# Kernel tuning notes

Hardware: AMD Instinct MI355X
Metric: run time of the kernel (lower is better)

The kernel has to match this reference:

```python
import jax, jax.numpy as jnp
import numpy as np

EMBED_DIM = 768
NUM_HEADS = 12
NUM_BOND_TYPES = 4
NEG_INF = -1e9


def setup_inputs() -> dict:
    key = jax.random.key(0)
    ks = jax.random.split(key, 8)
    B, N, E = 32, 512, EMBED_DIM
    x = jax.random.normal(ks[0], (B, N, E), dtype=jnp.float32)
    adj = jax.random.randint(ks[1], (B, N, N), 0, 2, dtype=jnp.int32)
    bond = jax.random.randint(ks[2], (B, N, N), 0, NUM_BOND_TYPES + 1, dtype=jnp.int32)
    # nn.Linear(E, 3E): weight (3E, E), bias (3E)
    lim_qkv = 1.0 / np.sqrt(E)
    qkv_w = jax.random.uniform(ks[3], (3 * E, E), minval=-lim_qkv, maxval=lim_qkv, dtype=jnp.float32)
    qkv_b = jax.random.uniform(ks[4], (3 * E,), minval=-lim_qkv, maxval=lim_qkv, dtype=jnp.float32)
    out_w = jax.random.uniform(ks[5], (E, E), minval=-lim_qkv, maxval=lim_qkv, dtype=jnp.float32)
    out_b = jax.random.uniform(ks[6], (E,), minval=-lim_qkv, maxval=lim_qkv, dtype=jnp.float32)
    # nn.Embedding(num_bond_types+1, 1), padding_idx=0 -> row 0 is zero
    bond_table = jax.random.normal(ks[7], (NUM_BOND_TYPES + 1, 1), dtype=jnp.float32)
    bond_table = bond_table.at[0].set(0.0)
    return {"x": x, "adj": adj, "bond": bond, "num_heads": NUM_HEADS,
            "qkv_w": qkv_w, "qkv_b": qkv_b, "out_w": out_w, "out_b": out_b,
            "bond_table": bond_table}


def reference(x, adj, bond, num_heads, qkv_w, qkv_b, out_w, out_b, bond_table):
    B, N, E = x.shape
    hd = E // num_heads
    scale = hd ** -0.5
    # enforce padding_idx=0 semantics
    bond_table = bond_table.at[0].set(0.0)
    qkv = x @ qkv_w.T + qkv_b                      # (B, N, 3E)
    qkv = qkv.reshape(B, N, 3, num_heads, hd).transpose(2, 0, 3, 1, 4)
    q, k, v = qkv[0], qkv[1], qkv[2]               # (B, h, N, hd)
    attn = jnp.einsum('bhnd,bhmd->bhnm', q, k) * scale
    attn = attn + adj.astype(x.dtype)[:, None, :, :]
    bond_bias = bond_table[bond, 0]                # (B, N, N) embedding gather
    attn = attn + bond_bias[:, None, :, :]
    attn = jnp.where(attn == 0, NEG_INF, attn)     # masked_fill(attn == 0)
    attn = jax.nn.softmax(attn, axis=-1)
    out = jnp.einsum('bhnm,bhmd->bhnd', attn, v)   # (B, h, N, hd)
    out = out.transpose(0, 2, 1, 3).reshape(B, N, E)
    return out @ out_w.T + out_b
```

## Files before the change

kernel.cpp:

```cpp
#include <hip/hip_runtime.h>
#include <hip/hip_bf16.h>

typedef __attribute__((ext_vector_type(8))) short short8;
typedef __attribute__((ext_vector_type(4))) float f32x4;
typedef __attribute__((ext_vector_type(4))) unsigned int uint4v;
typedef __attribute__((ext_vector_type(4))) int int4v;

#define MFMA16(a,b,c) __builtin_amdgcn_mfma_f32_16x16x32_bf16((a),(b),(c),0,0,0)

#define GLOAD_LDS16(g, l) \
    __builtin_amdgcn_global_load_lds((const __attribute__((address_space(1))) void*)(g), \
                                     (__attribute__((address_space(3))) void*)(l), 16, 0, 0)

__device__ __forceinline__ unsigned short f2bf(float f){
    union { float f; unsigned int u; } c; c.f = f;
    unsigned int u = c.u;
    u = (u + 0x7fffu + ((u >> 16) & 1u)) >> 16;
    return (unsigned short)u;
}
__device__ __forceinline__ float bf2f(unsigned short s){
    union { unsigned int u; float f; } c; c.u = ((unsigned int)s) << 16;
    return c.f;
}

__device__ __forceinline__ unsigned int pack_split(float f){
    unsigned int u = __builtin_bit_cast(unsigned int, f);
    float hi = __builtin_bit_cast(float, u & 0xffff0000u);
    unsigned int rem = __builtin_bit_cast(unsigned int, f - hi);
    return __builtin_amdgcn_perm(rem, u, 0x07060302u);
}

__device__ __forceinline__ void unpack8(uint4v u0, uint4v u1, short8& hi, short8& lo){
    uint4v h, l;
    h[0] = __builtin_amdgcn_perm(u0[1], u0[0], 0x05040100u);
    h[1] = __builtin_amdgcn_perm(u0[3], u0[2], 0x05040100u);
    h[2] = __builtin_amdgcn_perm(u1[1], u1[0], 0x05040100u);
    h[3] = __builtin_amdgcn_perm(u1[3], u1[2], 0x05040100u);
    l[0] = __builtin_amdgcn_perm(u0[1], u0[0], 0x07060302u);
    l[1] = __builtin_amdgcn_perm(u0[3], u0[2], 0x07060302u);
    l[2] = __builtin_amdgcn_perm(u1[1], u1[0], 0x07060302u);
    l[3] = __builtin_amdgcn_perm(u1[3], u1[2], 0x07060302u);
    hi = __builtin_bit_cast(short8, h);
    lo = __builtin_bit_cast(short8, l);
}

__global__ void pack_x_kernel(const float* __restrict__ x, unsigned int* __restrict__ img){
    int tid = blockIdx.x * 256 + threadIdx.x;
    int m = tid / 192, k4 = (tid - m*192) * 4;
    f32x4 v = *(const f32x4*)(x + (size_t)m*768 + k4);
    uint4v p;
    #pragma unroll
    for (int j = 0; j < 4; ++j) p[j] = pack_split(v[j]);
    int mt = m >> 7, row = m & 127, kt = k4 >> 5, u = k4 & 31;
    size_t off = ((size_t)(mt*24 + kt))*16384 + row*128 + (size_t)((u*4) ^ ((row&7)<<4));
    *(uint4v*)((char*)img + off) = p;
}

__global__ void pack_w_kernel(const float* __restrict__ wsrc, unsigned int* __restrict__ img, int total){
    int tid = blockIdx.x * 256 + threadIdx.x;
    if (tid >= total) return;
    int n = tid / 192, k4 = (tid - n*192) * 4;
    f32x4 v = *(const f32x4*)(wsrc + (size_t)n*768 + k4);
    uint4v p;
    #pragma unroll
    for (int j = 0; j < 4; ++j){
        unsigned short hh = f2bf(v[j]);
        unsigned short ll = f2bf(v[j] - bf2f(hh));
        p[j] = (unsigned int)hh | ((unsigned int)ll << 16);
    }
    int jt = n >> 7, row = n & 127, kt = k4 >> 5, u = k4 & 31;
    size_t off = ((size_t)(jt*24 + kt))*16384 + row*128 + (size_t)((u*4) ^ ((row&7)<<4));
    *(uint4v*)((char*)img + off) = p;
}

__global__ void bias_kernel(const int* __restrict__ adj, const int* __restrict__ bond,
                            const float* __restrict__ table, float* __restrict__ biasC, int n4){
    int i = blockIdx.x * 256 + threadIdx.x;
    if (i >= n4) return;
    int4v a  = ((const int4v*)adj)[i];
    int4v bd = ((const int4v*)bond)[i];
    const float t1 = table[1], t2 = table[2], t3 = table[3], t4 = table[4];
    f32x4 o;
    #pragma unroll
    for (int j = 0; j < 4; ++j){
        int bv = bd[j];
        float tb = (bv == 1) ? t1 : (bv == 2) ? t2 : (bv == 3) ? t3 : (bv == 4) ? t4 : 0.0f;
        o[j] = (float)a[j] + tb;
    }
    ((f32x4*)biasC)[i] = o;
}

template<int EMODE>
__global__ __launch_bounds__(256, 3)
void gemm_img(const unsigned int* __restrict__ Aimg, const unsigned int* __restrict__ Bimg,
              const float* __restrict__ bias, int NT, int RPX,
              float* __restrict__ C, int N,
              unsigned int* __restrict__ qo, unsigned int* __restrict__ ko,
              unsigned int* __restrict__ vo)
{
    __shared__ unsigned int lds[8192];

    const int lin = blockIdx.x;
    const int xcd = lin & 7, idx = lin >> 3;
    const int grp  = idx / (RPX * 6);
    const int rem  = idx - grp * (RPX * 6);
    const int rowL = rem / 6, c6 = rem - rowL * 6;
    const int colT = grp * 6 + c6;
    const int mt = xcd * RPX + rowL;
    const int m0 = mt << 7, j0 = colT << 7;

    const int t = threadIdx.x, l = t & 63, w = t >> 6;
    const int c = l & 15, g = l >> 4;
    const int wr = (w >> 1) * 64, wc2 = (w & 1) * 64;

    const unsigned int* Ablk = Aimg + (size_t)mt   * NT * 4096;
    const unsigned int* Bblk = Bimg + (size_t)colT * NT * 4096;

    f32x4 acc[4][4] = {};

    for (int kt = 0; kt < NT; ++kt){
        const unsigned int* As = Ablk + kt*4096 + t*4;
        const unsigned int* Bs = Bblk + kt*4096 + t*4;
        unsigned int* Ad = lds + t*4;
        unsigned int* Bd = lds + 4096 + t*4;
        #pragma unroll
        for (int i = 0; i < 4; ++i){
            GLOAD_LDS16(As + i*1024, Ad + i*1024);
            GLOAD_LDS16(Bs + i*1024, Bd + i*1024);
        }
        __syncthreads();

        short8 bh[4], bl[4];
        #pragma unroll
        for (int fc = 0; fc < 4; ++fc){
            int row = wc2 + fc*16 + c;
            int sw = (row & 7) << 4;
            const char* p = (const char*)(lds + 4096) + row*128;
            uint4v u0 = *(const uint4v*)(p + ((g*32     ) ^ sw));
            uint4v u1 = *(const uint4v*)(p + ((g*32 + 16) ^ sw));
            unpack8(u0, u1, bh[fc], bl[fc]);
        }
        #pragma unroll
        for (int fr = 0; fr < 4; ++fr){
            int row = wr + fr*16 + c;
            int sw = (row & 7) << 4;
            const char* p = (const char*)lds + row*128;
            uint4v u0 = *(const uint4v*)(p + ((g*32     ) ^ sw));
            uint4v u1 = *(const uint4v*)(p + ((g*32 + 16) ^ sw));
            short8 ah, al;
            unpack8(u0, u1, ah, al);
            #pragma unroll
            for (int fc = 0; fc < 4; ++fc){
                acc[fr][fc] = MFMA16(ah, bh[fc], acc[fr][fc]);
                acc[fr][fc] = MFMA16(ah, bl[fc], acc[fr][fc]);
                acc[fr][fc] = MFMA16(al, bh[fc], acc[fr][fc]);
            }
        }
        __syncthreads();
    }

    #pragma unroll
    for (int fr = 0; fr < 4; ++fr){
        #pragma unroll
        for (int fc = 0; fc < 4; ++fc){
            #pragma unroll
            for (int r = 0; r < 4; ++r){
                int m = m0 + wr + fr*16 + g*4 + r;
                int j = j0 + wc2 + fc*16 + c;
                float val = acc[fr][fc][r] + bias[j];
                if constexpr (EMODE == 0){
                    C[(size_t)m * N + j] = val;
                } else {
                    int sec = j / 768;
                    int off = j - sec * 768;
                    int head = off >> 6, d = off & 63;
                    int bb = m >> 9, n = m & 511;
                    unsigned int packed = pack_split(val);
                    if (sec == 2) {
                        vo[(((size_t)bb * 12 + head) * 64 + d) * 512 + n] = packed;
                    } else {
                        unsigned int* dst = (sec == 0) ? qo : ko;
                        dst[(((size_t)bb * 12 + head) * 512 + n) * 64 + d] = packed;
                    }
                }
            }
        }
    }
}

__global__ __launch_bounds__(256, 3)
void attn_kernel(const unsigned int* __restrict__ qb,
                 const unsigned int* __restrict__ kb,
                 const unsigned int* __restrict__ vtb,
                 const float* __restrict__ biasC,
                 unsigned int* __restrict__ oimg)
{
    __shared__ unsigned int Kt[64 * 64];
    __shared__ unsigned int Vt[64 * 64];
    __shared__ unsigned int Pt[4][16 * 68];

    const int lin = blockIdx.x;
    const int xcd = lin & 7, m_ = lin >> 3;
    const int bgrp = m_ / 96, r_ = m_ - bgrp * 96;
    const int b = (bgrp << 3) | xcd;
    const int h = r_ >> 3, qt = r_ & 7;
    const int bh = b * 12 + h, q0 = qt * 64;

    const int t = threadIdx.x, l = t & 63, w = t >> 6;
    const int c = l & 15, g = l >> 4;

    const unsigned int* qp  = qb  + (size_t)bh * 512 * 64;
    const unsigned int* kp  = kb  + (size_t)bh * 512 * 64;
    const unsigned int* vtp = vtb + (size_t)bh * 64 * 512;

    short8 qh[2], ql[2];
    {
        int qrow = q0 + w*16 + c;
        #pragma unroll
        for (int ks = 0; ks < 2; ++ks){
            const unsigned int* p = qp + (size_t)qrow * 64 + ks*32 + g*8;
            uint4v u0 = *(const uint4v*)p;
            uint4v u1 = *(const uint4v*)(p + 4);
            unpack8(u0, u1, qh[ks], ql[ks]);
        }
    }

    f32x4 O[4] = {};
    float mrow[4] = {-3e38f, -3e38f, -3e38f, -3e38f};
    float lrow[4] = {0.f, 0.f, 0.f, 0.f};

    const int srow = t >> 2;
    const int scol = (t & 3) * 16;
    const int ssw  = (srow & 7) << 4;

    auto rdfrag = [&](const unsigned int* base, int row, int colb, short8& hi, short8& lo){
        int sw = (row & 7) << 4;
        const char* p = (const char*)base + row*256;
        uint4v u0 = *(const uint4v*)(p + ((colb     ) ^ sw));
        uint4v u1 = *(const uint4v*)(p + ((colb + 16) ^ sw));
        unpack8(u0, u1, hi, lo);
    };

    for (int kt = 0; kt < 8; ++kt){
        {
            const unsigned int* kg = kp  + (size_t)(kt*64 + srow) * 64 + scol;
            const unsigned int* vg = vtp + (size_t)srow * 512 + kt*64 + scol;
            #pragma unroll
            for (int i = 0; i < 4; ++i){
                uint4v a  = *(const uint4v*)(kg + 4*i);
                uint4v bx = *(const uint4v*)(vg + 4*i);
                int cb = (scol + 4*i) * 4;
                *(uint4v*)((char*)Kt + srow*256 + (cb ^ ssw)) = a;
                *(uint4v*)((char*)Vt + srow*256 + (cb ^ ssw)) = bx;
            }
        }
        __syncthreads();

        float bia[4][4];
        #pragma unroll
        for (int fc = 0; fc < 4; ++fc){
            #pragma unroll
            for (int r = 0; r < 4; ++r){
                int rr = q0 + w*16 + g*4 + r;
                int cc = kt*64 + fc*16 + c;
                bia[fc][r] = biasC[((size_t)b * 512 + rr) * 512 + cc];
            }
        }

        f32x4 S[4] = {};
        #pragma unroll
        for (int fc = 0; fc < 4; ++fc){
            short8 kbh0, kbl0, kbh1, kbl1;
            rdfrag(Kt, fc*16 + c,       g*32, kbh0, kbl0);
            rdfrag(Kt, fc*16 + c, 128 + g*32, kbh1, kbl1);
            __builtin_amdgcn_s_setprio(1);
            S[fc] = MFMA16(qh[0], kbh0, S[fc]);
            S[fc] = MFMA16(qh[0], kbl0, S[fc]);
            S[fc] = MFMA16(ql[0], kbh0, S[fc]);
            S[fc] = MFMA16(qh[1], kbh1, S[fc]);
            S[fc] = MFMA16(qh[1], kbl1, S[fc]);
            S[fc] = MFMA16(ql[1], kbh1, S[fc]);
            __builtin_amdgcn_s_setprio(0);
        }

        float sv[4][4];
        #pragma unroll
        for (int fc = 0; fc < 4; ++fc){
            #pragma unroll
            for (int r = 0; r < 4; ++r){
                float val = fmaf(S[fc][r], 0.125f, bia[fc][r]);
                if (val == 0.0f) val = -1e9f;
                sv[fc][r] = val;
            }
        }

        float pvreg[4][4];
        #pragma unroll
        for (int r = 0; r < 4; ++r){
            float mt = fmaxf(fmaxf(sv[0][r], sv[1][r]), fmaxf(sv[2][r], sv[3][r]));
            #pragma unroll
            for (int off = 1; off < 16; off <<= 1)
                mt = fmaxf(mt, __shfl_xor(mt, off, 16));
            float mn = fmaxf(mrow[r], mt);
            float corr = __expf(mrow[r] - mn);
            float rs = 0.0f;
            #pragma unroll
            for (int fc = 0; fc < 4; ++fc){
                float p = __expf(sv[fc][r] - mn);
                pvreg[fc][r] = p;
                rs += p;
            }
            #pragma unroll
            for (int off = 1; off < 16; off <<= 1)
                rs += __shfl_xor(rs, off, 16);
            lrow[r] = lrow[r] * corr + rs;
            mrow[r] = mn;
            #pragma unroll
            for (int hf = 0; hf < 4; ++hf)
                O[hf][r] *= corr;
        }

        #pragma unroll
        for (int fc = 0; fc < 4; ++fc){
            #pragma unroll
            for (int r = 0; r < 4; ++r){
                Pt[w][(g*4 + r)*68 + fc*16 + c] = pack_split(pvreg[fc][r]);
            }
        }

        #pragma unroll
        for (int ks = 0; ks < 2; ++ks){
            const unsigned int* pp = &Pt[w][c*68 + ks*32 + g*8];
            uint4v pu0 = *(const uint4v*)pp;
            uint4v pu1 = *(const uint4v*)(pp + 4);
            short8 pah, pal;
            unpack8(pu0, pu1, pah, pal);
            #pragma unroll
            for (int hf = 0; hf < 4; ++hf){
                short8 vbh, vbl;
                rdfrag(Vt, hf*16 + c, ks*128 + g*32, vbh, vbl);
                __builtin_amdgcn_s_setprio(1);
                O[hf] = MFMA16(pah, vbh, O[hf]);
                O[hf] = MFMA16(pah, vbl, O[hf]);
                O[hf] = MFMA16(pal, vbh, O[hf]);
                __builtin_amdgcn_s_setprio(0);
            }
        }
        __syncthreads();
    }

    #pragma unroll
    for (int r = 0; r < 4; ++r){
        float inv = 1.0f / lrow[r];
        int m = b*512 + q0 + w*16 + g*4 + r;
        int mt = m >> 7, mrow2 = m & 127;
        int swz = (mrow2 & 7) << 4;
        size_t rowbase = ((size_t)mt*24)*16384 + (size_t)mrow2*128;
        #pragma unroll
        for (int hf = 0; hf < 4; ++hf){
            int e = h*64 + hf*16 + c;
            int kt2 = e >> 5, u = e & 31;
            size_t off = rowbase + (size_t)kt2*16384 + (size_t)((u*4) ^ swz);
            *(unsigned int*)((char*)oimg + off) = pack_split(O[hf][r] * inv);
        }
    }
}

extern "C" void kernel_launch(void* const* d_in, const int* in_sizes, int n_in,
                              void* d_out, int out_size, void* d_ws, size_t ws_size,
                              hipStream_t stream)
{
    const float* x     = (const float*)d_in[0];
    const int*   adj   = (const int*)d_in[1];
    const int*   bond  = (const int*)d_in[2];
    const float* qkv_w = (const float*)d_in[4];
    const float* qkv_b = (const float*)d_in[5];
    const float* out_w = (const float*)d_in[6];
    const float* out_b = (const float*)d_in[7];
    const float* btab  = (const float*)d_in[8];
    float* out = (float*)d_out;

    const size_t QKV = 12582912;
    unsigned int* q   = (unsigned int*)d_ws;
    unsigned int* k   = q  + QKV;
    unsigned int* vt  = k  + QKV;
    unsigned int* r1  = vt + QKV;
    unsigned int* w2i = r1 + QKV;
    unsigned int* r2  = w2i + 589824;
    unsigned int* w1i = r2;
    float* biasC      = (float*)r2;

    dim3 blk(256);
    pack_w_kernel<<<dim3(1728), blk, 0, stream>>>(qkv_w, w1i, 2304*192);
    pack_w_kernel<<<dim3(576),  blk, 0, stream>>>(out_w, w2i, 768*192);
    pack_x_kernel<<<dim3(12288), blk, 0, stream>>>(x, r1);

    gemm_img<1><<<dim3(2304), blk, 0, stream>>>(r1, w1i, qkv_b, 24, 16,
                                                nullptr, 2304, q, k, vt);

    bias_kernel<<<dim3(8192), blk, 0, stream>>>(adj, bond, btab, biasC, (32*512*512)/4);

    attn_kernel<<<dim3(3072), blk, 0, stream>>>(q, k, vt, biasC, r1);

    gemm_img<0><<<dim3(768), blk, 0, stream>>>(r1, w2i, out_b, 24, 16,
                                               out, 768, nullptr, nullptr, nullptr);
}
```

Baseline: 437.1 us.

## Fuse adjacency/bond bias into attention and pre-swizzle K/V tiles for direct LDS loads

Removes the separate bias kernel and its fp32 bias buffer. The attention kernel now reads the adj and bond int arrays directly and does the table lookup inline. The QKV GEMM epilogue writes K and V in a per-64-row tile layout that is already swizzled, so attention can copy them with global_load_lds straight into shared memory instead of going through registers. Each attention block (12 heads × 8 query tiles per batch) re-reads the adj/bond ints, where before it read a precomputed float bias. The total is two int reads per element instead of one float read, plus extra select arithmetic.

```diff
diff --git a/kernel.cpp b/kernel.cpp
--- a/kernel.cpp
+++ b/kernel.cpp
@@ -73,23 +73,6 @@
     *(uint4v*)((char*)img + off) = p;
 }
 
-__global__ void bias_kernel(const int* __restrict__ adj, const int* __restrict__ bond,
-                            const float* __restrict__ table, float* __restrict__ biasC, int n4){
-    int i = blockIdx.x * 256 + threadIdx.x;
-    if (i >= n4) return;
-    int4v a  = ((const int4v*)adj)[i];
-    int4v bd = ((const int4v*)bond)[i];
-    const float t1 = table[1], t2 = table[2], t3 = table[3], t4 = table[4];
-    f32x4 o;
-    #pragma unroll
-    for (int j = 0; j < 4; ++j){
-        int bv = bd[j];
-        float tb = (bv == 1) ? t1 : (bv == 2) ? t2 : (bv == 3) ? t3 : (bv == 4) ? t4 : 0.0f;
-        o[j] = (float)a[j] + tb;
-    }
-    ((f32x4*)biasC)[i] = o;
-}
-
 template<int EMODE>
 __global__ __launch_bounds__(256, 3)
 void gemm_img(const unsigned int* __restrict__ Aimg, const unsigned int* __restrict__ Bimg,
@@ -175,12 +158,18 @@
                     int off = j - sec * 768;
                     int head = off >> 6, d = off & 63;
                     int bb = m >> 9, n = m & 511;
+                    int bh2 = bb * 12 + head;
                     unsigned int packed = pack_split(val);
-                    if (sec == 2) {
-                        vo[(((size_t)bb * 12 + head) * 64 + d) * 512 + n] = packed;
+                    if (sec == 0) {
+                        qo[((size_t)bh2 * 512 + n) * 64 + d] = packed;
+                    } else if (sec == 1) {
+                        int row = n & 63;
+                        ko[(size_t)(bh2*8 + (n>>6))*4096 + row*64
+                           + (((d<<2) ^ ((row&7)<<4)) >> 2)] = packed;
                     } else {
-                        unsigned int* dst = (sec == 0) ? qo : ko;
-                        dst[(((size_t)bb * 12 + head) * 512 + n) * 64 + d] = packed;
+                        int col = n & 63;
+                        vo[(size_t)(bh2*8 + (n>>6))*4096 + d*64
+                           + (((col<<2) ^ ((d&7)<<4)) >> 2)] = packed;
                     }
                 }
             }
@@ -190,13 +179,15 @@
 
 __global__ __launch_bounds__(256, 3)
 void attn_kernel(const unsigned int* __restrict__ qb,
-                 const unsigned int* __restrict__ kb,
-                 const unsigned int* __restrict__ vtb,
-                 const float* __restrict__ biasC,
+                 const unsigned int* __restrict__ kimg,
+                 const unsigned int* __restrict__ vimg,
+                 const int* __restrict__ adj,
+                 const int* __restrict__ bond,
+                 const float* __restrict__ table,
                  unsigned int* __restrict__ oimg)
 {
-    __shared__ unsigned int Kt[64 * 64];
-    __shared__ unsigned int Vt[64 * 64];
+    __shared__ unsigned int Kt[4096];
+    __shared__ unsigned int Vt[4096];
     __shared__ unsigned int Pt[4][16 * 68];
 
     const int lin = blockIdx.x;
@@ -209,9 +200,8 @@
     const int t = threadIdx.x, l = t & 63, w = t >> 6;
     const int c = l & 15, g = l >> 4;
 
-    const unsigned int* qp  = qb  + (size_t)bh * 512 * 64;
-    const unsigned int* kp  = kb  + (size_t)bh * 512 * 64;
-    const unsigned int* vtp = vtb + (size_t)bh * 64 * 512;
+    const unsigned int* qp = qb + (size_t)bh * 512 * 64;
+    const float t1 = table[1], t2 = table[2], t3 = table[3], t4 = table[4];
 
     short8 qh[2], ql[2];
     {
@@ -228,10 +218,6 @@
     f32x4 O[4] = {};
     float mrow[4] = {-3e38f, -3e38f, -3e38f, -3e38f};
     float lrow[4] = {0.f, 0.f, 0.f, 0.f};
-
-    const int srow = t >> 2;
-    const int scol = (t & 3) * 16;
-    const int ssw  = (srow & 7) << 4;
 
     auto rdfrag = [&](const unsigned int* base, int row, int colb, short8& hi, short8& lo){
         int sw = (row & 7) << 4;
@@ -243,29 +229,28 @@
 
     for (int kt = 0; kt < 8; ++kt){
         {
-            const unsigned int* kg = kp  + (size_t)(kt*64 + srow) * 64 + scol;
-            const unsigned int* vg = vtp + (size_t)srow * 512 + kt*64 + scol;
+            const unsigned int* kg = kimg + (size_t)(bh*8 + kt)*4096 + t*4;
+            const unsigned int* vg = vimg + (size_t)(bh*8 + kt)*4096 + t*4;
             #pragma unroll
             for (int i = 0; i < 4; ++i){
-                uint4v a  = *(const uint4v*)(kg + 4*i);
-                uint4v bx = *(const uint4v*)(vg + 4*i);
-                int cb = (scol + 4*i) * 4;
-                *(uint4v*)((char*)Kt + srow*256 + (cb ^ ssw)) = a;
-                *(uint4v*)((char*)Vt + srow*256 + (cb ^ ssw)) = bx;
-            }
-        }
-        __syncthreads();
-
-        float bia[4][4];
+                GLOAD_LDS16(kg + i*1024, &Kt[t*4 + i*1024]);
+                GLOAD_LDS16(vg + i*1024, &Vt[t*4 + i*1024]);
+            }
+        }
+
+        int av[4][4], bv[4][4];
         #pragma unroll
         for (int fc = 0; fc < 4; ++fc){
             #pragma unroll
             for (int r = 0; r < 4; ++r){
                 int rr = q0 + w*16 + g*4 + r;
                 int cc = kt*64 + fc*16 + c;
-                bia[fc][r] = biasC[((size_t)b * 512 + rr) * 512 + cc];
-            }
-        }
+                size_t idx = ((size_t)b * 512 + rr) * 512 + cc;
+                av[fc][r] = adj[idx];
+                bv[fc][r] = bond[idx];
+            }
+        }
+        __syncthreads();
 
         f32x4 S[4] = {};
         #pragma unroll
@@ -288,7 +273,9 @@
         for (int fc = 0; fc < 4; ++fc){
             #pragma unroll
             for (int r = 0; r < 4; ++r){
-                float val = fmaf(S[fc][r], 0.125f, bia[fc][r]);
+                int bb2 = bv[fc][r];
+                float tb = (bb2 == 1) ? t1 : (bb2 == 2) ? t2 : (bb2 == 3) ? t3 : (bb2 == 4) ? t4 : 0.0f;
+                float val = fmaf(S[fc][r], 0.125f, (float)av[fc][r] + tb);
                 if (val == 0.0f) val = -1e9f;
                 sv[fc][r] = val;
             }
@@ -386,9 +373,7 @@
     unsigned int* vt  = k  + QKV;
     unsigned int* r1  = vt + QKV;
     unsigned int* w2i = r1 + QKV;
-    unsigned int* r2  = w2i + 589824;
-    unsigned int* w1i = r2;
-    float* biasC      = (float*)r2;
+    unsigned int* w1i = w2i + 589824;
 
     dim3 blk(256);
     pack_w_kernel<<<dim3(1728), blk, 0, stream>>>(qkv_w, w1i, 2304*192);
@@ -398,9 +383,7 @@
     gemm_img<1><<<dim3(2304), blk, 0, stream>>>(r1, w1i, qkv_b, 24, 16,
                                                 nullptr, 2304, q, k, vt);
 
-    bias_kernel<<<dim3(8192), blk, 0, stream>>>(adj, bond, btab, biasC, (32*512*512)/4);
-
-    attn_kernel<<<dim3(3072), blk, 0, stream>>>(q, k, vt, biasC, r1);
+    attn_kernel<<<dim3(3072), blk, 0, stream>>>(q, k, vt, adj, bond, btab, r1);
 
     gemm_img<0><<<dim3(768), blk, 0, stream>>>(r1, w2i, out_b, 24, 16,
                                                out, 768, nullptr, nullptr, nullptr);
```

Measured after the change: 451.6 us. +3.3%, slower.

## Store bf16 hi/lo planes pre-split in tiled images, drop in-kernel unpacking

Applied to the files above, without the earlier changes.

Every packed operand image (x, weights, Q/K/V, attention output) now keeps the bf16 high and low halves as separate 16-byte planes rather than interleaved pairs. The GEMM and attention kernels can then read MFMA fragments directly from LDS with no perm-based unpacking. K and V are written by the QKV GEMM epilogue as pre-swizzled 64x64 tiles, so attention loads them with direct global-to-LDS copies instead of register staging. The bias loads now overlap those copies, and s_setprio is added around the GEMM MFMAs; the cost is scattered 2-byte stores in the epilogues.

```diff
diff --git a/kernel.cpp b/kernel.cpp
--- a/kernel.cpp
+++ b/kernel.cpp
@@ -21,6 +21,13 @@
 __device__ __forceinline__ float bf2f(unsigned short s){
     union { unsigned int u; float f; } c; c.u = ((unsigned int)s) << 16;
     return c.f;
+}
+
+__device__ __forceinline__ void tsplit(float f, unsigned short &h, unsigned short &l){
+    unsigned int u = __builtin_bit_cast(unsigned int, f);
+    float hi = __builtin_bit_cast(float, u & 0xffff0000u);
+    h = (unsigned short)(u >> 16);
+    l = (unsigned short)(__builtin_bit_cast(unsigned int, f - hi) >> 16);
 }
 
 __device__ __forceinline__ unsigned int pack_split(float f){
@@ -44,33 +51,47 @@
     lo = __builtin_bit_cast(short8, l);
 }
 
+
 __global__ void pack_x_kernel(const float* __restrict__ x, unsigned int* __restrict__ img){
     int tid = blockIdx.x * 256 + threadIdx.x;
-    int m = tid / 192, k4 = (tid - m*192) * 4;
-    f32x4 v = *(const f32x4*)(x + (size_t)m*768 + k4);
-    uint4v p;
+    int m = tid / 96, grp = tid - m * 96;
+    const float* src = x + (size_t)m * 768 + grp * 8;
+    f32x4 v0 = ((const f32x4*)src)[0];
+    f32x4 v1 = ((const f32x4*)src)[1];
+    short8 h8, l8;
     #pragma unroll
-    for (int j = 0; j < 4; ++j) p[j] = pack_split(v[j]);
-    int mt = m >> 7, row = m & 127, kt = k4 >> 5, u = k4 & 31;
-    size_t off = ((size_t)(mt*24 + kt))*16384 + row*128 + (size_t)((u*4) ^ ((row&7)<<4));
-    *(uint4v*)((char*)img + off) = p;
+    for (int j = 0; j < 4; ++j){
+        unsigned short hh, ll;
+        tsplit(v0[j], hh, ll); h8[j]   = (short)hh; l8[j]   = (short)ll;
+        tsplit(v1[j], hh, ll); h8[4+j] = (short)hh; l8[4+j] = (short)ll;
+    }
+    int mt = m >> 7, row = m & 127, kt = grp >> 2, gi = grp & 3;
+    int sw = (row & 7) << 4;
+    char* bp = (char*)img + ((size_t)(mt*24 + kt))*16384 + row*128;
+    *(short8*)(bp + ((gi*32     ) ^ sw)) = h8;
+    *(short8*)(bp + ((gi*32 + 16) ^ sw)) = l8;
 }
 
 __global__ void pack_w_kernel(const float* __restrict__ wsrc, unsigned int* __restrict__ img, int total){
     int tid = blockIdx.x * 256 + threadIdx.x;
     if (tid >= total) return;
-    int n = tid / 192, k4 = (tid - n*192) * 4;
-    f32x4 v = *(const f32x4*)(wsrc + (size_t)n*768 + k4);
-    uint4v p;
+    int n = tid / 96, grp = tid - n * 96;
+    const float* src = wsrc + (size_t)n * 768 + grp * 8;
+    f32x4 v0 = ((const f32x4*)src)[0];
+    f32x4 v1 = ((const f32x4*)src)[1];
+    short8 h8, l8;
     #pragma unroll
     for (int j = 0; j < 4; ++j){
-        unsigned short hh = f2bf(v[j]);
-        unsigned short ll = f2bf(v[j] - bf2f(hh));
-        p[j] = (unsigned int)hh | ((unsigned int)ll << 16);
-    }
-    int jt = n >> 7, row = n & 127, kt = k4 >> 5, u = k4 & 31;
-    size_t off = ((size_t)(jt*24 + kt))*16384 + row*128 + (size_t)((u*4) ^ ((row&7)<<4));
-    *(uint4v*)((char*)img + off) = p;
+        unsigned short hh = f2bf(v0[j]);
+        h8[j] = (short)hh; l8[j] = (short)f2bf(v0[j] - bf2f(hh));
+        hh = f2bf(v1[j]);
+        h8[4+j] = (short)hh; l8[4+j] = (short)f2bf(v1[j] - bf2f(hh));
+    }
+    int jt = n >> 7, row = n & 127, kt = grp >> 2, gi = grp & 3;
+    int sw = (row & 7) << 4;
+    char* bp = (char*)img + ((size_t)(jt*24 + kt))*16384 + row*128;
+    *(short8*)(bp + ((gi*32     ) ^ sw)) = h8;
+    *(short8*)(bp + ((gi*32 + 16) ^ sw)) = l8;
 }
 
 __global__ void bias_kernel(const int* __restrict__ adj, const int* __restrict__ bond,
@@ -95,8 +116,7 @@
 void gemm_img(const unsigned int* __restrict__ Aimg, const unsigned int* __restrict__ Bimg,
               const float* __restrict__ bias, int NT, int RPX,
               float* __restrict__ C, int N,
-              unsigned int* __restrict__ qo, unsigned int* __restrict__ ko,
-              unsigned int* __restrict__ vo)
+              char* __restrict__ qo, char* __restrict__ ko, char* __restrict__ vo)
 {
     __shared__ unsigned int lds[8192];
 
@@ -136,25 +156,24 @@
             int row = wc2 + fc*16 + c;
             int sw = (row & 7) << 4;
             const char* p = (const char*)(lds + 4096) + row*128;
-            uint4v u0 = *(const uint4v*)(p + ((g*32     ) ^ sw));
-            uint4v u1 = *(const uint4v*)(p + ((g*32 + 16) ^ sw));
-            unpack8(u0, u1, bh[fc], bl[fc]);
+            bh[fc] = *(const short8*)(p + ((g*32     ) ^ sw));
+            bl[fc] = *(const short8*)(p + ((g*32 + 16) ^ sw));
         }
         #pragma unroll
         for (int fr = 0; fr < 4; ++fr){
             int row = wr + fr*16 + c;
             int sw = (row & 7) << 4;
             const char* p = (const char*)lds + row*128;
-            uint4v u0 = *(const uint4v*)(p + ((g*32     ) ^ sw));
-            uint4v u1 = *(const uint4v*)(p + ((g*32 + 16) ^ sw));
-            short8 ah, al;
-            unpack8(u0, u1, ah, al);
+            short8 ah = *(const short8*)(p + ((g*32     ) ^ sw));
+            short8 al = *(const short8*)(p + ((g*32 + 16) ^ sw));
+            __builtin_amdgcn_s_setprio(1);
             #pragma unroll
             for (int fc = 0; fc < 4; ++fc){
                 acc[fr][fc] = MFMA16(ah, bh[fc], acc[fr][fc]);
                 acc[fr][fc] = MFMA16(ah, bl[fc], acc[fr][fc]);
                 acc[fr][fc] = MFMA16(al, bh[fc], acc[fr][fc]);
             }
+            __builtin_amdgcn_s_setprio(0);
         }
         __syncthreads();
     }
@@ -175,12 +194,23 @@
                     int off = j - sec * 768;
                     int head = off >> 6, d = off & 63;
                     int bb = m >> 9, n = m & 511;
-                    unsigned int packed = pack_split(val);
-                    if (sec == 2) {
-                        vo[(((size_t)bb * 12 + head) * 64 + d) * 512 + n] = packed;
+                    int bh2 = bb * 12 + head;
+                    unsigned short hh, ll;
+                    tsplit(val, hh, ll);
+                    if (sec == 0) {
+                        char* p = qo + ((size_t)bh2*512 + n)*256 + (d>>3)*32 + (d&7)*2;
+                        *(unsigned short*)(p     ) = hh;
+                        *(unsigned short*)(p + 16) = ll;
+                    } else if (sec == 1) {
+                        int row = n & 63, sw = (row & 7) << 4;
+                        char* p = ko + (size_t)(bh2*8 + (n>>6))*16384 + row*256;
+                        *(unsigned short*)(p + ((((d>>3)*32)     ) ^ sw) + (d&7)*2) = hh;
+                        *(unsigned short*)(p + ((((d>>3)*32) + 16) ^ sw) + (d&7)*2) = ll;
                     } else {
-                        unsigned int* dst = (sec == 0) ? qo : ko;
-                        dst[(((size_t)bb * 12 + head) * 512 + n) * 64 + d] = packed;
+                        int col = n & 63, sw = (d & 7) << 4;
+                        char* p = vo + (size_t)(bh2*8 + (n>>6))*16384 + d*256;
+                        *(unsigned short*)(p + ((((col>>3)*32)     ) ^ sw) + (col&7)*2) = hh;
+                        *(unsigned short*)(p + ((((col>>3)*32) + 16) ^ sw) + (col&7)*2) = ll;
                     }
                 }
             }
@@ -189,14 +219,14 @@
 }
 
 __global__ __launch_bounds__(256, 3)
-void attn_kernel(const unsigned int* __restrict__ qb,
-                 const unsigned int* __restrict__ kb,
-                 const unsigned int* __restrict__ vtb,
+void attn_kernel(const char* __restrict__ qb,
+                 const unsigned int* __restrict__ kimg,
+                 const unsigned int* __restrict__ vimg,
                  const float* __restrict__ biasC,
-                 unsigned int* __restrict__ oimg)
+                 char* __restrict__ oimg)
 {
-    __shared__ unsigned int Kt[64 * 64];
-    __shared__ unsigned int Vt[64 * 64];
+    __shared__ unsigned int Kt[4096];
+    __shared__ unsigned int Vt[4096];
     __shared__ unsigned int Pt[4][16 * 68];
 
     const int lin = blockIdx.x;
@@ -209,19 +239,14 @@
     const int t = threadIdx.x, l = t & 63, w = t >> 6;
     const int c = l & 15, g = l >> 4;
 
-    const unsigned int* qp  = qb  + (size_t)bh * 512 * 64;
-    const unsigned int* kp  = kb  + (size_t)bh * 512 * 64;
-    const unsigned int* vtp = vtb + (size_t)bh * 64 * 512;
-
     short8 qh[2], ql[2];
     {
         int qrow = q0 + w*16 + c;
+        const char* qp = qb + ((size_t)bh*512 + qrow)*256;
         #pragma unroll
         for (int ks = 0; ks < 2; ++ks){
-            const unsigned int* p = qp + (size_t)qrow * 64 + ks*32 + g*8;
-            uint4v u0 = *(const uint4v*)p;
-            uint4v u1 = *(const uint4v*)(p + 4);
-            unpack8(u0, u1, qh[ks], ql[ks]);
+            qh[ks] = *(const short8*)(qp + ks*128 + g*32);
+            ql[ks] = *(const short8*)(qp + ks*128 + g*32 + 16);
         }
     }
 
@@ -229,32 +254,23 @@
     float mrow[4] = {-3e38f, -3e38f, -3e38f, -3e38f};
     float lrow[4] = {0.f, 0.f, 0.f, 0.f};
 
-    const int srow = t >> 2;
-    const int scol = (t & 3) * 16;
-    const int ssw  = (srow & 7) << 4;
-
     auto rdfrag = [&](const unsigned int* base, int row, int colb, short8& hi, short8& lo){
         int sw = (row & 7) << 4;
         const char* p = (const char*)base + row*256;
-        uint4v u0 = *(const uint4v*)(p + ((colb     ) ^ sw));
-        uint4v u1 = *(const uint4v*)(p + ((colb + 16) ^ sw));
-        unpack8(u0, u1, hi, lo);
+        hi = *(const short8*)(p + ((colb     ) ^ sw));
+        lo = *(const short8*)(p + ((colb + 16) ^ sw));
     };
 
     for (int kt = 0; kt < 8; ++kt){
         {
-            const unsigned int* kg = kp  + (size_t)(kt*64 + srow) * 64 + scol;
-            const unsigned int* vg = vtp + (size_t)srow * 512 + kt*64 + scol;
+            const unsigned int* kg = kimg + (size_t)(bh*8 + kt)*4096 + t*4;
+            const unsigned int* vg = vimg + (size_t)(bh*8 + kt)*4096 + t*4;
             #pragma unroll
             for (int i = 0; i < 4; ++i){
-                uint4v a  = *(const uint4v*)(kg + 4*i);
-                uint4v bx = *(const uint4v*)(vg + 4*i);
-                int cb = (scol + 4*i) * 4;
-                *(uint4v*)((char*)Kt + srow*256 + (cb ^ ssw)) = a;
-                *(uint4v*)((char*)Vt + srow*256 + (cb ^ ssw)) = bx;
-            }
-        }
-        __syncthreads();
+                GLOAD_LDS16(kg + i*1024, &Kt[t*4 + i*1024]);
+                GLOAD_LDS16(vg + i*1024, &Vt[t*4 + i*1024]);
+            }
+        }
 
         float bia[4][4];
         #pragma unroll
@@ -266,6 +282,7 @@
                 bia[fc][r] = biasC[((size_t)b * 512 + rr) * 512 + cc];
             }
         }
+        __syncthreads();
 
         f32x4 S[4] = {};
         #pragma unroll
@@ -355,13 +372,16 @@
         int m = b*512 + q0 + w*16 + g*4 + r;
         int mt = m >> 7, mrow2 = m & 127;
         int swz = (mrow2 & 7) << 4;
-        size_t rowbase = ((size_t)mt*24)*16384 + (size_t)mrow2*128;
+        char* rowp = oimg + ((size_t)mt*24)*16384 + (size_t)mrow2*128;
         #pragma unroll
         for (int hf = 0; hf < 4; ++hf){
             int e = h*64 + hf*16 + c;
-            int kt2 = e >> 5, u = e & 31;
-            size_t off = rowbase + (size_t)kt2*16384 + (size_t)((u*4) ^ swz);
-            *(unsigned int*)((char*)oimg + off) = pack_split(O[hf][r] * inv);
+            int kt2 = e >> 5, gi = (e >> 3) & 3, pos = e & 7;
+            unsigned short hh, ll;
+            tsplit(O[hf][r] * inv, hh, ll);
+            char* p = rowp + (size_t)kt2*16384;
+            *(unsigned short*)(p + (((gi*32)     ) ^ swz) + pos*2) = hh;
+            *(unsigned short*)(p + (((gi*32) + 16) ^ swz) + pos*2) = ll;
         }
     }
 }
@@ -391,16 +411,16 @@
     float* biasC      = (float*)r2;
 
     dim3 blk(256);
-    pack_w_kernel<<<dim3(1728), blk, 0, stream>>>(qkv_w, w1i, 2304*192);
-    pack_w_kernel<<<dim3(576),  blk, 0, stream>>>(out_w, w2i, 768*192);
-    pack_x_kernel<<<dim3(12288), blk, 0, stream>>>(x, r1);
+    pack_w_kernel<<<dim3(864), blk, 0, stream>>>(qkv_w, w1i, 2304*96);
+    pack_w_kernel<<<dim3(288), blk, 0, stream>>>(out_w, w2i, 768*96);
+    pack_x_kernel<<<dim3(6144), blk, 0, stream>>>(x, r1);
 
     gemm_img<1><<<dim3(2304), blk, 0, stream>>>(r1, w1i, qkv_b, 24, 16,
-                                                nullptr, 2304, q, k, vt);
+                                                nullptr, 2304, (char*)q, (char*)k, (char*)vt);
 
     bias_kernel<<<dim3(8192), blk, 0, stream>>>(adj, bond, btab, biasC, (32*512*512)/4);
 
-    attn_kernel<<<dim3(3072), blk, 0, stream>>>(q, k, vt, biasC, r1);
+    attn_kernel<<<dim3(3072), blk, 0, stream>>>((const char*)q, k, vt, biasC, (char*)r1);
 
     gemm_img<0><<<dim3(768), blk, 0, stream>>>(r1, w2i, out_b, 24, 16,
                                                out, 768, nullptr, nullptr, nullptr);
```

Result: faster. 415.4 us (-5.0%).
